# Kernel optimization log

Measured on AMD Instinct MI355X. Metric: run time of the kernel, lower is better.

Reference implementation:

```python
import jax, jax.numpy as jnp
import numpy as np


def setup_inputs() -> dict:
    key = jax.random.key(0)
    ks = jax.random.split(key, 10)
    b, n, d = 4, 64, 64
    E = 4096
    node_emb = jax.random.normal(ks[0], (b * n, d), dtype=jnp.float32)
    path_emb = jax.random.normal(ks[1], (b, n, n, d), dtype=jnp.float32)
    edge_index = jax.random.randint(ks[2], (2, E), 0, b * n, dtype=jnp.int64)
    # learned params, stored as (in, out) so application is x @ W + b
    W_hz = jax.random.normal(ks[3], (d, d), dtype=jnp.float32) / np.sqrt(d)
    b_hz = jnp.zeros((d,), dtype=jnp.float32)
    W_zz = jax.random.normal(ks[4], (3 * d, d), dtype=jnp.float32) / np.sqrt(3 * d)
    b_zz = jnp.zeros((d,), dtype=jnp.float32)
    W_nm = jax.random.normal(ks[5], (2 * d, d), dtype=jnp.float32) / np.sqrt(2 * d)
    b_nm = jnp.zeros((d,), dtype=jnp.float32)
    return {
        "node_emb": node_emb, "path_emb": path_emb, "edge_index": edge_index,
        "W_hz": W_hz, "b_hz": b_hz, "W_zz": W_zz, "b_zz": b_zz,
        "W_nm": W_nm, "b_nm": b_nm,
    }


def reference(node_emb, path_emb, edge_index, W_hz, b_hz, W_zz, b_zz, W_nm, b_nm):
    b, n, _, d = path_emb.shape
    # ---- PathConv (aggr='max') ----
    z = path_emb @ W_hz + b_hz                                  # (b, n, n, d)
    # tropical (max-plus) matmul over paths: z_conv[b,i,j,d] = max_k z[b,i,k,d] + z[b,k,j,d]
    z_conv = jnp.max(z[:, :, :, None, :] + z[:, None, :, :, :], axis=2)  # (b, n, n, d)
    z = jnp.maximum(z_conv, z)                                  # path_aggr mode='max'
    ne = node_emb.reshape(b, n, d)
    n_i = jnp.broadcast_to(ne[:, :, None, :], (b, n, n, d))
    n_j = jnp.broadcast_to(ne[:, None, :, :], (b, n, n, d))
    u_path = jax.nn.relu(jnp.concatenate([n_i, z, n_j], axis=-1) @ W_zz + b_zz)
    # ---- MPLayer (default message = x_j, aggr='add'; edge_attr unused) ----
    src, dst = edge_index[0], edge_index[1]
    aggr_msg = jax.ops.segment_sum(node_emb[src], dst, num_segments=node_emb.shape[0])
    u_node = jax.nn.relu(jnp.concatenate([node_emb, aggr_msg], axis=-1) @ W_nm + b_nm)
    # residual
    return (u_node + node_emb, u_path + path_emb)
```

## Files before the change

### kernel.cpp

```cpp
#include <hip/hip_runtime.h>


__global__ __launch_bounds__(256) void k_pathlin(
    const float* __restrict__ pe, const float* __restrict__ Whz,
    const float* __restrict__ bhz, float* __restrict__ zt) {
  int blk = blockIdx.x;
  int bi = blk >> 2, q = blk & 3;
  int b = bi >> 6, i = bi & 63;
  int t = threadIdx.x, lane = t & 63, g = t >> 6;
  __shared__ float sA[16][64];
  __shared__ float sB[64][64];
  ((float4*)sA)[t] = ((const float4*)(pe + (size_t)bi * 4096 + q * 1024))[t];
  {
    const float4* W4 = (const float4*)Whz;
    float4* sB4 = (float4*)sB;
#pragma unroll
    for (int it = 0; it < 4; ++it) sB4[t + 256 * it] = W4[t + 256 * it];
  }
  __syncthreads();
  float bv = bhz[lane];
  float acc[4] = {bv, bv, bv, bv};
  int kl0 = g * 4;
  for (int c = 0; c < 64; c += 4) {
    float w0 = sB[c + 0][lane], w1 = sB[c + 1][lane];
    float w2 = sB[c + 2][lane], w3 = sB[c + 3][lane];
#pragma unroll
    for (int kk = 0; kk < 4; ++kk) {
      const float4 p = *(const float4*)&sA[kl0 + kk][c];
      acc[kk] += p.x * w0 + p.y * w1 + p.z * w2 + p.w * w3;
    }
  }
  float* dst = zt + (size_t)b * 262144 + (size_t)lane * 4096
             + (size_t)i * 64 + q * 16 + kl0;
  *(float4*)dst = make_float4(acc[0], acc[1], acc[2], acc[3]);
}

__global__ __launch_bounds__(256) void k_trop_node(
    const float* __restrict__ zt, float* __restrict__ zt2,
    const float* __restrict__ ne, const int* __restrict__ eidx,
    const float* __restrict__ Wzz, const float* __restrict__ Wnm,
    const float* __restrict__ bnm,
    float* __restrict__ a1, float* __restrict__ a3, float* __restrict__ out0) {
  int t = threadIdx.x, lane = t & 63, g = t >> 6;
  __shared__ float A[64][64];
  __shared__ float part[4][64];
  __shared__ float nlal[2][64];
  if (blockIdx.x < 1024) {
    int slice = blockIdx.x >> 2, iq = blockIdx.x & 3;
    const float4* s4 = (const float4*)(zt + (size_t)slice * 4096);
    float4* d4 = (float4*)&A[0][0];
#pragma unroll
    for (int it = 0; it < 4; ++it) d4[t + 256 * it] = s4[t + 256 * it];
    __syncthreads();
    int j = lane, i0 = iq * 16 + g * 4;
    float acc[4];
#pragma unroll
    for (int ii = 0; ii < 4; ++ii) acc[ii] = A[i0 + ii][j];
    for (int k = 0; k < 64; k += 4) {
      float b0 = A[k + 0][j], b1 = A[k + 1][j];
      float b2 = A[k + 2][j], b3 = A[k + 3][j];
#pragma unroll
      for (int ii = 0; ii < 4; ++ii) {
        const float4 a = *(const float4*)&A[i0 + ii][k];
        float m0 = fmaxf(a.x + b0, a.y + b1);
        float m1 = fmaxf(a.z + b2, a.w + b3);
        acc[ii] = fmaxf(acc[ii], fmaxf(m0, m1));
      }
    }
    float* Og = zt2 + (size_t)slice * 4096;
#pragma unroll
    for (int ii = 0; ii < 4; ++ii) Og[(i0 + ii) * 64 + j] = acc[ii];
  } else {
    int r = blockIdx.x - 1024;
    int* elist = (int*)&A[0][0];
    const int* srcv = eidx;
    const int* dstv = eidx + 4096;
    int cntw = 0;
    unsigned long long ltmask = (lane == 63) ? 0x7fffffffffffffffull
                                             : ((1ull << lane) - 1ull);
    for (int q = 0; q < 16; ++q) {
      int e2 = g * 1024 + q * 64 + lane;
      bool match = (dstv[e2] == r);
      unsigned long long mask = __ballot(match);
      if (match) {
        int pos = cntw + __popcll(mask & ltmask);
        elist[g * 1024 + pos] = srcv[e2];
      }
      cntw += __popcll(mask);
    }
    float accA = 0.f;
    for (int m = 0; m < cntw; ++m) accA += ne[elist[g * 1024 + m] * 64 + lane];
    part[g][lane] = accA;
    if (g == 0) nlal[0][lane] = ne[r * 64 + lane];
    __syncthreads();
    if (g == 0)
      nlal[1][lane] = part[0][lane] + part[1][lane] + part[2][lane] + part[3][lane];
    __syncthreads();
    float s = 0.f;
    for (int d2 = g * 16; d2 < g * 16 + 16; ++d2) {
      s += nlal[0][d2] * Wnm[d2 * 64 + lane]
         + nlal[1][d2] * Wnm[(64 + d2) * 64 + lane];
    }
    part[g][lane] = s;
    if (g == 0) {
      const float* nr = ne + r * 64;
      float s1 = 0.f;
      for (int d2 = 0; d2 < 64; ++d2) s1 += nr[d2] * Wzz[d2 * 64 + lane];
      a1[r * 64 + lane] = s1;
    } else if (g == 1) {
      const float* nr = ne + r * 64;
      float s3 = 0.f;
      for (int d2 = 0; d2 < 64; ++d2) s3 += nr[d2] * Wzz[(128 + d2) * 64 + lane];
      a3[r * 64 + lane] = s3;
    }
    __syncthreads();
    if (g == 0) {
      float v = part[0][lane] + part[1][lane] + part[2][lane] + part[3][lane]
                + bnm[lane];
      v = fmaxf(v, 0.f);
      out0[r * 64 + lane] = v + nlal[0][lane];
    }
  }
}

__global__ __launch_bounds__(256) void k_upath(
    const float* __restrict__ zt2, const float* __restrict__ Wzz,
    const float* __restrict__ bzz, const float* __restrict__ a1,
    const float* __restrict__ a3, const float* __restrict__ pe,
    float* __restrict__ out1) {
  int blk = blockIdx.x;
  int bi = blk >> 2, jq = blk & 3;
  int b = bi >> 6, i = bi & 63;
  int t = threadIdx.x, lane = t & 63, g = t >> 6;
  __shared__ float W2[64][64];
  __shared__ float sZ[64][16];
  {
    const float4* W4 = (const float4*)(Wzz + 4096);
    float4* W24 = (float4*)W2;
#pragma unroll
    for (int it = 0; it < 4; ++it) W24[t + 256 * it] = W4[t + 256 * it];
  }
  {
    int d2 = t >> 2, c4 = t & 3;
    const float* src = zt2 + (size_t)b * 262144 + (size_t)d2 * 4096
                     + (size_t)i * 64 + jq * 16 + c4 * 4;
    *(float4*)&sZ[d2][c4 * 4] = *(const float4*)src;
  }
  __syncthreads();
  int e = lane;
  float base = a1[bi * 64 + e] + bzz[e];
  float acc[4] = {base, base, base, base};
  for (int d2 = 0; d2 < 64; ++d2) {
    float w = W2[d2][e];
    const float4 z4 = *(const float4*)&sZ[d2][g * 4];
    acc[0] += z4.x * w;
    acc[1] += z4.y * w;
    acc[2] += z4.z * w;
    acc[3] += z4.w * w;
  }
  const float* a3b = a3 + (size_t)(b * 64) * 64;
  size_t obase = (size_t)bi * 4096;
#pragma unroll
  for (int jj = 0; jj < 4; ++jj) {
    int j = jq * 16 + g * 4 + jj;
    float v = acc[jj] + a3b[j * 64 + e];
    v = fmaxf(v, 0.f);
    out1[obase + j * 64 + e] = v + pe[obase + j * 64 + e];
  }
}

extern "C" void kernel_launch(void* const* d_in, const int* in_sizes, int n_in,
                              void* d_out, int out_size, void* d_ws, size_t ws_size,
                              hipStream_t stream) {
  const float* node = (const float*)d_in[0];
  const float* pe   = (const float*)d_in[1];
  const int*   eidx = (const int*)d_in[2];
  const float* Whz  = (const float*)d_in[3];
  const float* bhz  = (const float*)d_in[4];
  const float* Wzz  = (const float*)d_in[5];
  const float* bzz  = (const float*)d_in[6];
  const float* Wnm  = (const float*)d_in[7];
  const float* bnm  = (const float*)d_in[8];
  float* out0 = (float*)d_out;
  float* out1 = out0 + 16384;
  float* zt  = (float*)d_ws;
  float* a1  = zt + 1048576;
  float* a3  = a1 + 16384;
  float* zt2 = a3 + 16384;

  hipLaunchKernelGGL(k_pathlin, dim3(1024), dim3(256), 0, stream, pe, Whz, bhz, zt);
  hipLaunchKernelGGL(k_trop_node, dim3(1280), dim3(256), 0, stream,
                     zt, zt2, node, eidx, Wzz, Wnm, bnm, a1, a3, out0);
  hipLaunchKernelGGL(k_upath, dim3(1024), dim3(256), 0, stream,
                     zt2, Wzz, bzz, a1, a3, pe, out1);
}
```

Measured before the change: 31.45 us.

## Replace LDS staging with register-held operands and wave-uniform scalar loads

Result: slower. 39.09 us (+24.3%).

```diff
diff --git a/kernel.cpp b/kernel.cpp
--- a/kernel.cpp
+++ b/kernel.cpp
@@ -1,5 +1,7 @@
 #include <hip/hip_runtime.h>
 
+
+__device__ __forceinline__ int rfl(int x) { return __builtin_amdgcn_readfirstlane(x); }
 
 __global__ __launch_bounds__(256) void k_pathlin(
     const float* __restrict__ pe, const float* __restrict__ Whz,
@@ -7,32 +9,25 @@
   int blk = blockIdx.x;
   int bi = blk >> 2, q = blk & 3;
   int b = bi >> 6, i = bi & 63;
-  int t = threadIdx.x, lane = t & 63, g = t >> 6;
-  __shared__ float sA[16][64];
-  __shared__ float sB[64][64];
-  ((float4*)sA)[t] = ((const float4*)(pe + (size_t)bi * 4096 + q * 1024))[t];
-  {
-    const float4* W4 = (const float4*)Whz;
-    float4* sB4 = (float4*)sB;
+  int t = threadIdx.x, lane = t & 63;
+  int g = rfl(t >> 6);
+  float wreg[64];
 #pragma unroll
-    for (int it = 0; it < 4; ++it) sB4[t + 256 * it] = W4[t + 256 * it];
-  }
-  __syncthreads();
+  for (int c = 0; c < 64; ++c) wreg[c] = Whz[c * 64 + lane];
+  const float* rowbase = pe + (size_t)bi * 4096 + (size_t)(q * 16 + g * 4) * 64;
   float bv = bhz[lane];
-  float acc[4] = {bv, bv, bv, bv};
-  int kl0 = g * 4;
-  for (int c = 0; c < 64; c += 4) {
-    float w0 = sB[c + 0][lane], w1 = sB[c + 1][lane];
-    float w2 = sB[c + 2][lane], w3 = sB[c + 3][lane];
+  float acc0 = bv, acc1 = bv, acc2 = bv, acc3 = bv;
 #pragma unroll
-    for (int kk = 0; kk < 4; ++kk) {
-      const float4 p = *(const float4*)&sA[kl0 + kk][c];
-      acc[kk] += p.x * w0 + p.y * w1 + p.z * w2 + p.w * w3;
-    }
+  for (int c = 0; c < 64; ++c) {
+    float w = wreg[c];
+    acc0 += rowbase[c] * w;
+    acc1 += rowbase[64 + c] * w;
+    acc2 += rowbase[128 + c] * w;
+    acc3 += rowbase[192 + c] * w;
   }
   float* dst = zt + (size_t)b * 262144 + (size_t)lane * 4096
-             + (size_t)i * 64 + q * 16 + kl0;
-  *(float4*)dst = make_float4(acc[0], acc[1], acc[2], acc[3]);
+             + (size_t)i * 64 + q * 16 + g * 4;
+  *(float4*)dst = make_float4(acc0, acc1, acc2, acc3);
 }
 
 __global__ __launch_bounds__(256) void k_trop_node(
@@ -41,38 +36,39 @@
     const float* __restrict__ Wzz, const float* __restrict__ Wnm,
     const float* __restrict__ bnm,
     float* __restrict__ a1, float* __restrict__ a3, float* __restrict__ out0) {
-  int t = threadIdx.x, lane = t & 63, g = t >> 6;
-  __shared__ float A[64][64];
+  int t = threadIdx.x, lane = t & 63;
+  int g = rfl(t >> 6);
+  __shared__ float shA[4][1024];
   __shared__ float part[4][64];
   __shared__ float nlal[2][64];
   if (blockIdx.x < 1024) {
     int slice = blockIdx.x >> 2, iq = blockIdx.x & 3;
-    const float4* s4 = (const float4*)(zt + (size_t)slice * 4096);
-    float4* d4 = (float4*)&A[0][0];
+    const float* Ag = zt + (size_t)slice * 4096;
+    float colreg[64];
 #pragma unroll
-    for (int it = 0; it < 4; ++it) d4[t + 256 * it] = s4[t + 256 * it];
-    __syncthreads();
-    int j = lane, i0 = iq * 16 + g * 4;
-    float acc[4];
+    for (int k = 0; k < 64; ++k) colreg[k] = Ag[k * 64 + lane];
+    int i0 = iq * 16 + g * 4;
+    const float* rb = Ag + (size_t)i0 * 64;
+    float acc0 = rb[lane];
+    float acc1 = rb[64 + lane];
+    float acc2 = rb[128 + lane];
+    float acc3 = rb[192 + lane];
 #pragma unroll
-    for (int ii = 0; ii < 4; ++ii) acc[ii] = A[i0 + ii][j];
-    for (int k = 0; k < 64; k += 4) {
-      float b0 = A[k + 0][j], b1 = A[k + 1][j];
-      float b2 = A[k + 2][j], b3 = A[k + 3][j];
-#pragma unroll
-      for (int ii = 0; ii < 4; ++ii) {
-        const float4 a = *(const float4*)&A[i0 + ii][k];
-        float m0 = fmaxf(a.x + b0, a.y + b1);
-        float m1 = fmaxf(a.z + b2, a.w + b3);
-        acc[ii] = fmaxf(acc[ii], fmaxf(m0, m1));
-      }
+    for (int k = 0; k < 64; ++k) {
+      float c = colreg[k];
+      acc0 = fmaxf(acc0, rb[k] + c);
+      acc1 = fmaxf(acc1, rb[64 + k] + c);
+      acc2 = fmaxf(acc2, rb[128 + k] + c);
+      acc3 = fmaxf(acc3, rb[192 + k] + c);
     }
-    float* Og = zt2 + (size_t)slice * 4096;
-#pragma unroll
-    for (int ii = 0; ii < 4; ++ii) Og[(i0 + ii) * 64 + j] = acc[ii];
+    float* Og = zt2 + (size_t)slice * 4096 + (size_t)i0 * 64;
+    Og[lane] = acc0;
+    Og[64 + lane] = acc1;
+    Og[128 + lane] = acc2;
+    Og[192 + lane] = acc3;
   } else {
     int r = blockIdx.x - 1024;
-    int* elist = (int*)&A[0][0];
+    int* elist = (int*)&shA[0][0];
     const int* srcv = eidx;
     const int* dstv = eidx + 4096;
     int cntw = 0;
@@ -131,41 +127,32 @@
   int blk = blockIdx.x;
   int bi = blk >> 2, jq = blk & 3;
   int b = bi >> 6, i = bi & 63;
-  int t = threadIdx.x, lane = t & 63, g = t >> 6;
-  __shared__ float W2[64][64];
-  __shared__ float sZ[64][16];
-  {
-    const float4* W4 = (const float4*)(Wzz + 4096);
-    float4* W24 = (float4*)W2;
+  int t = threadIdx.x, lane = t & 63;
+  int g = rfl(t >> 6);
+  float w2[64];
 #pragma unroll
-    for (int it = 0; it < 4; ++it) W24[t + 256 * it] = W4[t + 256 * it];
-  }
-  {
-    int d2 = t >> 2, c4 = t & 3;
-    const float* src = zt2 + (size_t)b * 262144 + (size_t)d2 * 4096
-                     + (size_t)i * 64 + jq * 16 + c4 * 4;
-    *(float4*)&sZ[d2][c4 * 4] = *(const float4*)src;
-  }
-  __syncthreads();
-  int e = lane;
-  float base = a1[bi * 64 + e] + bzz[e];
-  float acc[4] = {base, base, base, base};
-  for (int d2 = 0; d2 < 64; ++d2) {
-    float w = W2[d2][e];
-    const float4 z4 = *(const float4*)&sZ[d2][g * 4];
-    acc[0] += z4.x * w;
-    acc[1] += z4.y * w;
-    acc[2] += z4.z * w;
-    acc[3] += z4.w * w;
+  for (int d = 0; d < 64; ++d) w2[d] = Wzz[(64 + d) * 64 + lane];
+  int j0 = jq * 16 + g * 4;
+  const float* zb = zt2 + (size_t)b * 262144 + (size_t)i * 64 + j0;
+  float base = a1[bi * 64 + lane] + bzz[lane];
+  float acc0 = base, acc1 = base, acc2 = base, acc3 = base;
+#pragma unroll
+  for (int d = 0; d < 64; ++d) {
+    const float* zd = zb + (size_t)d * 4096;
+    float w = w2[d];
+    acc0 += zd[0] * w;
+    acc1 += zd[1] * w;
+    acc2 += zd[2] * w;
+    acc3 += zd[3] * w;
   }
   const float* a3b = a3 + (size_t)(b * 64) * 64;
-  size_t obase = (size_t)bi * 4096;
+  size_t ob = (size_t)bi * 4096 + (size_t)j0 * 64;
+  float acc[4] = {acc0, acc1, acc2, acc3};
 #pragma unroll
   for (int jj = 0; jj < 4; ++jj) {
-    int j = jq * 16 + g * 4 + jj;
-    float v = acc[jj] + a3b[j * 64 + e];
+    float v = acc[jj] + a3b[(j0 + jj) * 64 + lane];
     v = fmaxf(v, 0.f);
-    out1[obase + j * 64 + e] = v + pe[obase + j * 64 + e];
+    out1[ob + jj * 64 + lane] = v + pe[ob + jj * 64 + lane];
   }
 }
 
```
